# Kernel tuning notes

Measured on AMD Instinct MI355X. Metric: run time of the kernel, lower is better.

Reference implementation:

```python
import jax, jax.numpy as jnp
import numpy as np

N_NODES = 50000
N_EDGES = 800000
NODE_DIM = 64
EDGE_DIM = 16
HIDDEN = 128
EPS = 1e-5


def _linear_init(key, fan_in, fan_out):
    k1, k2 = jax.random.split(key)
    bound = 1.0 / np.sqrt(fan_in)
    W = jax.random.uniform(k1, (fan_in, fan_out), minval=-bound, maxval=bound, dtype=jnp.float32)
    b = jax.random.uniform(k2, (fan_out,), minval=-bound, maxval=bound, dtype=jnp.float32)
    return W, b


def batchnorm(h, gamma, beta):
    # BatchNorm1d in training mode: batch mean/var (biased), eps=1e-5
    mu = jnp.mean(h, axis=0, keepdims=True)
    var = jnp.mean((h - mu) ** 2, axis=0, keepdims=True)
    return (h - mu) * jax.lax.rsqrt(var + EPS) * gamma + beta


def setup_inputs() -> dict:
    key = jax.random.key(0)
    ks = jax.random.split(key, 8)
    x = jax.random.normal(ks[0], (N_NODES, NODE_DIM), dtype=jnp.float32)
    edge_index = jax.random.randint(ks[1], (2, N_EDGES), 0, N_NODES, dtype=jnp.int64)
    edge_attr = jax.random.normal(ks[2], (N_EDGES, EDGE_DIM), dtype=jnp.float32)
    We1, be1 = _linear_init(ks[3], 2 * NODE_DIM + EDGE_DIM, HIDDEN)
    We2, be2 = _linear_init(ks[4], HIDDEN, HIDDEN)
    Wm, bm = _linear_init(ks[5], HIDDEN, HIDDEN)
    Wn1, bn1 = _linear_init(ks[6], NODE_DIM + HIDDEN, HIDDEN)
    Wn2, bn2 = _linear_init(ks[7], HIDDEN, HIDDEN)
    ones = jnp.ones((HIDDEN,), jnp.float32)
    zeros = jnp.zeros((HIDDEN,), jnp.float32)
    return dict(x=x, edge_index=edge_index, edge_attr=edge_attr,
                We1=We1, be1=be1, ge=ones, bbe=zeros, We2=We2, be2=be2,
                Wm=Wm, bm=bm,
                Wn1=Wn1, bn1=bn1, gn=ones, bbn=zeros, Wn2=Wn2, bn2=bn2)


def reference(x, edge_index, edge_attr, We1, be1, ge, bbe, We2, be2, Wm, bm, Wn1, bn1, gn, bbn, Wn2, bn2):
    row, col = edge_index[0], edge_index[1]
    # gather + concat -> edge network (Linear, BN, ReLU, Linear)
    edge_input = jnp.concatenate([x[row], x[col], edge_attr], axis=-1)  # [E, 2n+e]
    h = jax.nn.relu(batchnorm(edge_input @ We1 + be1, ge, bbe))
    edge_features = h @ We2 + be2
    # message MLP (Linear, ReLU)
    messages = jax.nn.relu(edge_features @ Wm + bm)  # [E, H]
    # scatter-add into source nodes
    agg = jax.ops.segment_sum(messages, row, num_segments=N_NODES)  # [N, H]
    # node network (Linear, BN, ReLU, Linear)
    node_input = jnp.concatenate([x, agg], axis=-1)
    hn = jax.nn.relu(batchnorm(node_input @ Wn1 + bn1, gn, bbn))
    return hn @ Wn2 + bn2
```

## Files before the change

### kernel.cpp

```cpp
#include <hip/hip_runtime.h>
#include <stdint.h>

#define NNODES 50000
#define NEDGES 800000
#define H 128
#define BN_EPS 1e-5f

typedef short short8 __attribute__((ext_vector_type(8)));
typedef short short4v __attribute__((ext_vector_type(4)));
typedef float f32x4 __attribute__((ext_vector_type(4)));

__device__ __forceinline__ float bf2f(unsigned short u) {
    unsigned int v = ((unsigned int)u) << 16;
    return __uint_as_float(v);
}
__device__ __forceinline__ unsigned short f2bf(float f) {
    unsigned int x = __float_as_uint(f);
    return (unsigned short)((x + 0x7FFFu + ((x >> 16) & 1u)) >> 16);
}
__device__ __forceinline__ short8 s8z() { short8 z = {0,0,0,0,0,0,0,0}; return z; }

template<int KB>
__device__ __forceinline__ void gemm_tile(const short* __restrict__ sA, const int SK,
                                          const unsigned short* __restrict__ WT, const int RK,
                                          const int n0, f32x4 acc[4][4], const int lane) {
    const int mr = lane & 15, quad = lane >> 4;
    const short* W = (const short*)WT;
    #pragma unroll
    for (int kb = 0; kb < KB; ++kb) {
        short8 a[4];
        #pragma unroll
        for (int mt = 0; mt < 4; ++mt)
            a[mt] = *(const short8*)&sA[(mt*16 + mr)*SK + kb*32 + quad*8];
        #pragma unroll
        for (int nt = 0; nt < 4; ++nt) {
            short8 b = *(const short8*)&W[(size_t)(n0 + nt*16 + mr)*RK + kb*32 + quad*8];
            #pragma unroll
            for (int mt = 0; mt < 4; ++mt)
                acc[mt][nt] = __builtin_amdgcn_mfma_f32_16x16x32_bf16(a[mt], b, acc[mt][nt], 0, 0, 0);
        }
    }
}

__global__ void k_fold(const float* __restrict__ We2, const float* __restrict__ be2,
                       const float* __restrict__ Wm, const float* __restrict__ bm,
                       float* __restrict__ W2m, float* __restrict__ b2m) {
    int j = threadIdx.x;
    int i = blockIdx.x;
    if (i < H) {
        float acc = 0.f;
        for (int k = 0; k < H; ++k) acc = fmaf(We2[i*H + k], Wm[k*H + j], acc);
        W2m[i*H + j] = acc;
    } else {
        float acc = bm[j];
        for (int k = 0; k < H; ++k) acc = fmaf(be2[k], Wm[k*H + j], acc);
        b2m[j] = acc;
    }
}

__global__ void k_prep2(const float* __restrict__ We1, const float* __restrict__ Wn1,
                        const float* __restrict__ Wn2,
                        unsigned short* __restrict__ WabT, unsigned short* __restrict__ Wn1T,
                        unsigned short* __restrict__ Wn2T, unsigned short* __restrict__ WcT,
                        int* __restrict__ cnt, float* __restrict__ S1f) {
    int i = blockIdx.x*256 + threadIdx.x;
    if (i < 16384) {
        int n = i >> 6, k = i & 63;
        WabT[n*64 + k] = f2bf(We1[(n < 128 ? k : 64 + k)*H + (n & 127)]);
    } else if (i < 40960) {
        int j = i - 16384; int n = j / 192, k = j - n*192;
        Wn1T[n*192 + k] = f2bf(Wn1[k*H + n]);
    } else if (i < 57344) {
        int j = i - 40960; int n = j >> 7, k = j & 127;
        Wn2T[n*H + k] = f2bf(Wn2[k*H + n]);
    } else if (i < 61440) {
        int j = i - 57344; int n = j >> 5, k = j & 31;
        WcT[n*32 + k] = (k < 16) ? f2bf(We1[(128 + k)*H + n]) : (unsigned short)0;
    } else if (i < 111440) {
        cnt[i - 61440] = 0;
    } else if (i < 112464) {
        S1f[i - 111440] = 0.f;
    }
}

__global__ void k_count(const int* __restrict__ ei, int* __restrict__ cnt) {
    int e = blockIdx.x*256 + threadIdx.x;
    if (e < NEDGES) atomicAdd(&cnt[ei[e]], 1);
}

__global__ void k_scanA(const int* __restrict__ cnt, int* __restrict__ bsum) {
    __shared__ int ws[4];
    const int tid = threadIdx.x;
    int i = blockIdx.x*256 + tid;
    int v = (i < NNODES) ? cnt[i] : 0;
    #pragma unroll
    for (int off = 32; off > 0; off >>= 1) v += __shfl_down(v, off);
    if ((tid & 63) == 0) ws[tid >> 6] = v;
    __syncthreads();
    if (tid == 0) bsum[blockIdx.x] = ws[0] + ws[1] + ws[2] + ws[3];
}

__global__ void k_scanB(const int* __restrict__ bsum, int* __restrict__ bpre,
                        int* __restrict__ offsets) {
    __shared__ int ws[4];
    const int tid = threadIdx.x;
    const int lane = tid & 63, wid = tid >> 6;
    int v = (tid < 196) ? bsum[tid] : 0;
    int xv = v;
    #pragma unroll
    for (int off = 1; off < 64; off <<= 1) {
        int y = __shfl_up(xv, off);
        if (lane >= off) xv += y;
    }
    if (lane == 63) ws[wid] = xv;
    __syncthreads();
    int base = 0;
    for (int w = 0; w < 4; ++w) if (w < wid) base += ws[w];
    int incl = base + xv;
    if (tid < 196) bpre[tid] = incl - v;
    if (tid == 255) offsets[NNODES] = incl;
}

__global__ void k_scanC(const int* __restrict__ cnt, const int* __restrict__ bpre,
                        int* __restrict__ offsets, int* __restrict__ cursor) {
    __shared__ int ws[4];
    const int tid = threadIdx.x;
    const int lane = tid & 63, wid = tid >> 6;
    int i = blockIdx.x*256 + tid;
    int v = (i < NNODES) ? cnt[i] : 0;
    int xv = v;
    #pragma unroll
    for (int off = 1; off < 64; off <<= 1) {
        int y = __shfl_up(xv, off);
        if (lane >= off) xv += y;
    }
    if (lane == 63) ws[wid] = xv;
    __syncthreads();
    int base = bpre[blockIdx.x];
    for (int w = 0; w < 4; ++w) if (w < wid) base += ws[w];
    int excl = base + xv - v;
    if (i < NNODES) { offsets[i] = excl; cursor[i] = excl; }
}

__global__ void k_scatter(const int* __restrict__ ei, int* __restrict__ cursor,
                          int* __restrict__ elist) {
    int e = blockIdx.x*256 + threadIdx.x;
    if (e < NEDGES) {
        int p = atomicAdd(&cursor[ei[e]], 1);
        elist[p] = e;
    }
}

__launch_bounds__(256)
__global__ void k_T(const float* __restrict__ x, const unsigned short* __restrict__ WabT,
                    unsigned short* __restrict__ T) {
    __shared__ short sA[128*72];
    const int tid = threadIdx.x;
    const int n0b = blockIdx.x*128;
    {
        const int rowl = tid >> 1, half = (tid & 1)*32;
        const int node = n0b + rowl;
        const bool ok = node < NNODES;
        #pragma unroll
        for (int c = 0; c < 4; ++c) {
            int k0 = half + c*8;
            short8 o = s8z();
            if (ok) {
                float4 a = *(const float4*)&x[node*64 + k0];
                float4 b = *(const float4*)&x[node*64 + k0 + 4];
                o[0]=(short)f2bf(a.x); o[1]=(short)f2bf(a.y); o[2]=(short)f2bf(a.z); o[3]=(short)f2bf(a.w);
                o[4]=(short)f2bf(b.x); o[5]=(short)f2bf(b.y); o[6]=(short)f2bf(b.z); o[7]=(short)f2bf(b.w);
            }
            *(short8*)&sA[rowl*72 + k0] = o;
        }
    }
    __syncthreads();
    const int wave = tid >> 6, lane = tid & 63;
    const int m0 = (wave & 1)*64;
    const int n0 = blockIdx.y*128 + (wave >> 1)*64;
    f32x4 acc[4][4];
    f32x4 z = {0.f, 0.f, 0.f, 0.f};
    #pragma unroll
    for (int mt = 0; mt < 4; ++mt)
        #pragma unroll
        for (int nt = 0; nt < 4; ++nt) acc[mt][nt] = z;
    gemm_tile<2>(sA + m0*72, 72, WabT, 64, n0, acc, lane);
    const int mr = lane & 15, quad = lane >> 4;
    #pragma unroll
    for (int nt = 0; nt < 4; ++nt) {
        int j = n0 + nt*16 + mr;
        #pragma unroll
        for (int mt = 0; mt < 4; ++mt) {
            int nb = n0b + m0 + mt*16 + quad*4;
            #pragma unroll
            for (int r = 0; r < 4; ++r) {
                int node = nb + r;
                if (node < NNODES) T[(size_t)node*256 + j] = f2bf(acc[mt][nt][r]);
            }
        }
    }
}

__launch_bounds__(256, 4)
__global__ void k_gather3(const unsigned short* __restrict__ T, const int* __restrict__ ei,
                          const int* __restrict__ elist, const float* __restrict__ ea,
                          const unsigned short* __restrict__ WcT, const float* __restrict__ be1,
                          unsigned short* __restrict__ hb,
                          float* __restrict__ gS, float* __restrict__ gSS) {
    __shared__ short sT[128*136];
    __shared__ float sS[H], sSS[H];
    const int tid = threadIdx.x;
    const int p0 = blockIdx.x*128;
    const int wave = tid >> 6, lane = tid & 63;
    const int mr = lane & 15, quad = lane >> 4;
    const int mbase = wave*32;
    if (tid < 128) { sS[tid] = 0.f; sSS[tid] = 0.f; }
    const int lp = tid >> 1, half = tid & 1;
    const int e = elist[p0 + lp];
    const bool eaActive = (quad < 2);
    int e0i = 0, e1i = 0;
    if (eaActive) {
        e0i = elist[p0 + mbase + mr];
        e1i = elist[p0 + mbase + 16 + mr];
    }
    const int row = ei[e], col = ei[NEDGES + e];
    f32x4 u0, u1, v0, v1;
    if (eaActive) {
        u0 = __builtin_nontemporal_load((const f32x4*)&ea[(size_t)e0i*16 + quad*8]);
        u1 = __builtin_nontemporal_load((const f32x4*)&ea[(size_t)e0i*16 + quad*8 + 4]);
        v0 = __builtin_nontemporal_load((const f32x4*)&ea[(size_t)e1i*16 + quad*8]);
        v1 = __builtin_nontemporal_load((const f32x4*)&ea[(size_t)e1i*16 + quad*8 + 4]);
    }
    const unsigned short* Tr = &T[(size_t)row*256 + half*64];
    const unsigned short* Tc = &T[(size_t)col*256 + 128 + half*64];
    short8 t1[8], t2[8];
    #pragma unroll
    for (int c = 0; c < 8; ++c) t1[c] = *(const short8*)&Tr[c*8];
    #pragma unroll
    for (int c = 0; c < 8; ++c) t2[c] = *(const short8*)&Tc[c*8];
    __builtin_amdgcn_sched_barrier(0);
    short8 a0 = s8z(), a1 = s8z();
    if (eaActive) {
        a0[0]=(short)f2bf(u0[0]); a0[1]=(short)f2bf(u0[1]); a0[2]=(short)f2bf(u0[2]); a0[3]=(short)f2bf(u0[3]);
        a0[4]=(short)f2bf(u1[0]); a0[5]=(short)f2bf(u1[1]); a0[6]=(short)f2bf(u1[2]); a0[7]=(short)f2bf(u1[3]);
        a1[0]=(short)f2bf(v0[0]); a1[1]=(short)f2bf(v0[1]); a1[2]=(short)f2bf(v0[2]); a1[3]=(short)f2bf(v0[3]);
        a1[4]=(short)f2bf(v1[0]); a1[5]=(short)f2bf(v1[1]); a1[6]=(short)f2bf(v1[2]); a1[7]=(short)f2bf(v1[3]);
    }
    #pragma unroll
    for (int c = 0; c < 8; ++c) {
        short8 o;
        #pragma unroll
        for (int i = 0; i < 8; ++i)
            o[i] = (short)f2bf(bf2f((unsigned short)t1[c][i]) + bf2f((unsigned short)t2[c][i]));
        *(short8*)&sT[lp*136 + half*64 + c*8] = o;
    }
    f32x4 acc[2][8];
    f32x4 z = {0.f, 0.f, 0.f, 0.f};
    #pragma unroll
    for (int mt = 0; mt < 2; ++mt)
        #pragma unroll
        for (int nt = 0; nt < 8; ++nt) acc[mt][nt] = z;
    #pragma unroll
    for (int nt = 0; nt < 8; ++nt) {
        short8 b = *(const short8*)&WcT[(nt*16 + mr)*32 + quad*8];
        acc[0][nt] = __builtin_amdgcn_mfma_f32_16x16x32_bf16(a0, b, acc[0][nt], 0, 0, 0);
        acc[1][nt] = __builtin_amdgcn_mfma_f32_16x16x32_bf16(a1, b, acc[1][nt], 0, 0, 0);
    }
    __syncthreads();
    #pragma unroll
    for (int nt = 0; nt < 8; ++nt) {
        int j = nt*16 + mr;
        float bia = be1[j];
        float s = 0.f, ssum = 0.f;
        #pragma unroll
        for (int mt = 0; mt < 2; ++mt) {
            #pragma unroll
            for (int r = 0; r < 4; ++r) {
                int m = mbase + mt*16 + quad*4 + r;
                float v = acc[mt][nt][r] + bf2f((unsigned short)sT[m*136 + j]) + bia;
                sT[m*136 + j] = (short)f2bf(v);
                s += v; ssum += v*v;
            }
        }
        s += __shfl_xor(s, 16);
        ssum += __shfl_xor(ssum, 16);
        s += __shfl_xor(s, 32);
        ssum += __shfl_xor(ssum, 32);
        if (quad == 0) {
            atomicAdd(&sS[j], s);
            atomicAdd(&sSS[j], ssum);
        }
    }
    __syncthreads();
    #pragma unroll
    for (int c = 0; c < 8; ++c) {
        int k0 = half*64 + c*8;
        int kb = k0 >> 5, quadS = (k0 >> 3) & 3;
        short8 v = *(const short8*)&sT[lp*136 + k0];
        __builtin_nontemporal_store(v,
            (short8*)&hb[((size_t)(blockIdx.x*16 + kb*4 + quadS)*128 + lp)*8]);
    }
    if (tid < 128) { atomicAdd(&gS[tid], sS[tid]); atomicAdd(&gSS[tid], sSS[tid]); }
}

__global__ void k_stats(const float* __restrict__ S, const float* __restrict__ SS,
                        const float* __restrict__ g, const float* __restrict__ b,
                        float invCount, float* __restrict__ scale, float* __restrict__ shift) {
    int j = threadIdx.x;
    float mu = S[j]*invCount;
    float var = SS[j]*invCount - mu*mu;
    float sc = rsqrtf(var + BN_EPS)*g[j];
    scale[j] = sc;
    shift[j] = b[j] - mu*sc;
}

__global__ void k_prep3(const float* __restrict__ W2m, const float* __restrict__ scale,
                        const float* __restrict__ shift, unsigned short* __restrict__ W2mST,
                        float* __restrict__ tvec, float* __restrict__ agg) {
    int i = blockIdx.x*256 + threadIdx.x;
    if (i < 16384) {
        int n = i >> 7, k = i & 127;
        W2mST[n*H + k] = f2bf(scale[k] * W2m[k*H + n]);
    } else if (i < 16512) {
        int k = i - 16384;
        tvec[k] = shift[k] / scale[k];
    } else if (i < 16512 + NNODES*H) {
        agg[i - 16512] = 0.f;
    }
}

__launch_bounds__(256)
__global__ void k_msgagg(const unsigned short* __restrict__ hb, const float* __restrict__ tvec,
                         const unsigned short* __restrict__ W2mST, const float* __restrict__ b2m,
                         const int* __restrict__ ei, const int* __restrict__ elist,
                         const int* __restrict__ offsets, float* __restrict__ agg) {
    __shared__ short sA[128*136];
    __shared__ int rows[128];
    __shared__ int segStart[130];
    __shared__ int wcnt[2];
    __shared__ int nsegS;
    const int tid = threadIdx.x;
    const int p0 = blockIdx.x*128;
    const int wave = tid >> 6, lane = tid & 63;
    const int mr = lane & 15, quad = lane >> 4;
    const int mbase = wave*32;
    short8 raw[4][2];
    #pragma unroll
    for (int kb = 0; kb < 4; ++kb)
        #pragma unroll
        for (int mt = 0; mt < 2; ++mt)
            raw[kb][mt] = __builtin_nontemporal_load(
                (const short8*)&hb[((size_t)(blockIdx.x*16 + kb*4 + quad)*128
                                    + mbase + mt*16 + mr)*8]);
    int pre = 0, st = 0;
    if (tid < 128) rows[tid] = ei[elist[p0 + tid]];
    __syncthreads();
    if (tid < 128) {
        int r0 = rows[tid];
        st = (tid == 0) || (rows[tid - 1] != r0);
        unsigned long long m = __ballot(st);
        int lane2 = tid & 63;
        pre = __popcll(m & ((1ull << lane2) - 1ull));
        if (lane2 == 63) wcnt[tid >> 6] = pre + st;
    }
    __syncthreads();
    if (tid < 128) {
        int base = (tid >= 64) ? wcnt[0] : 0;
        int sid = base + pre + st - 1;
        if (st) segStart[sid] = tid;
        if (tid == 127) {
            int ns = wcnt[0] + wcnt[1];
            nsegS = ns;
            segStart[ns] = 128;
        }
    }
    f32x4 acc[2][8];
    f32x4 z = {0.f, 0.f, 0.f, 0.f};
    #pragma unroll
    for (int mt = 0; mt < 2; ++mt)
        #pragma unroll
        for (int nt = 0; nt < 8; ++nt) acc[mt][nt] = z;
    #pragma unroll
    for (int kb = 0; kb < 4; ++kb) {
        float4 tq0 = *(const float4*)&tvec[kb*32 + quad*8];
        float4 tq1 = *(const float4*)&tvec[kb*32 + quad*8 + 4];
        short8 a[2];
        #pragma unroll
        for (int mt = 0; mt < 2; ++mt) {
            short8 rw = raw[kb][mt];
            short8 av;
            av[0] = (short)f2bf(fmaxf(bf2f((unsigned short)rw[0]) + tq0.x, 0.f));
            av[1] = (short)f2bf(fmaxf(bf2f((unsigned short)rw[1]) + tq0.y, 0.f));
            av[2] = (short)f2bf(fmaxf(bf2f((unsigned short)rw[2]) + tq0.z, 0.f));
            av[3] = (short)f2bf(fmaxf(bf2f((unsigned short)rw[3]) + tq0.w, 0.f));
            av[4] = (short)f2bf(fmaxf(bf2f((unsigned short)rw[4]) + tq1.x, 0.f));
            av[5] = (short)f2bf(fmaxf(bf2f((unsigned short)rw[5]) + tq1.y, 0.f));
            av[6] = (short)f2bf(fmaxf(bf2f((unsigned short)rw[6]) + tq1.z, 0.f));
            av[7] = (short)f2bf(fmaxf(bf2f((unsigned short)rw[7]) + tq1.w, 0.f));
            a[mt] = av;
        }
        #pragma unroll
        for (int nt = 0; nt < 8; ++nt) {
            short8 b = *(const short8*)&W2mST[(nt*16 + mr)*H + kb*32 + quad*8];
            acc[0][nt] = __builtin_amdgcn_mfma_f32_16x16x32_bf16(a[0], b, acc[0][nt], 0, 0, 0);
            acc[1][nt] = __builtin_amdgcn_mfma_f32_16x16x32_bf16(a[1], b, acc[1][nt], 0, 0, 0);
        }
    }
    #pragma unroll
    for (int nt = 0; nt < 8; ++nt) {
        int j = nt*16 + mr;
        float bias = b2m[j];
        #pragma unroll
        for (int mt = 0; mt < 2; ++mt) {
            #pragma unroll
            for (int r = 0; r < 4; ++r) {
                int m = mbase + mt*16 + quad*4 + r;
                sA[m*136 + j] = (short)f2bf(fmaxf(acc[mt][nt][r] + bias, 0.f));
            }
        }
    }
    __syncthreads();
    const int nseg = nsegS;
    for (int idx = tid; idx < (nseg << 5); idx += 256) {
        int s = idx >> 5, g = idx & 31;
        int j0 = g*4;
        int a0 = segStart[s], b0 = segStart[s + 1];
        float s0 = 0.f, s1 = 0.f, s2 = 0.f, s3 = 0.f;
        for (int i = a0; i < b0; ++i) {
            short4v v = *(const short4v*)&sA[i*136 + j0];
            s0 += bf2f((unsigned short)v[0]);
            s1 += bf2f((unsigned short)v[1]);
            s2 += bf2f((unsigned short)v[2]);
            s3 += bf2f((unsigned short)v[3]);
        }
        int r = rows[a0];
        bool interior = (a0 > 0) && (b0 < 128);
        bool full = interior || ((p0 + a0 == offsets[r]) && (p0 + b0 == offsets[r + 1]));
        float* dst = &agg[(size_t)r*H + j0];
        if (full) {
            f32x4 o = {s0, s1, s2, s3};
            *(f32x4*)dst = o;
        } else {
            atomicAdd(dst + 0, s0);
            atomicAdd(dst + 1, s1);
            atomicAdd(dst + 2, s2);
            atomicAdd(dst + 3, s3);
        }
    }
}

__launch_bounds__(256)
__global__ void k_node1(const float* __restrict__ x, const float* __restrict__ agg,
                        const unsigned short* __restrict__ Wn1T, const float* __restrict__ bn1,
                        float* __restrict__ h2, float* __restrict__ gS, float* __restrict__ gSS) {
    __shared__ short sA[128*200];
    __shared__ float sS[H], sSS[H];
    const int tid = threadIdx.x;
    if (tid < H) { sS[tid] = 0.f; sSS[tid] = 0.f; }
    const int n0b = blockIdx.x*128;
    {
        const int rowl = tid >> 1, half = (tid & 1)*96;
        const int node = n0b + rowl;
        const bool ok = node < NNODES;
        #pragma unroll
        for (int c = 0; c < 12; ++c) {
            int k0 = half + c*8;
            short8 o = s8z();
            if (ok) {
                float4 a, b;
                if (k0 < 64) {
                    a = *(const float4*)&x[node*64 + k0];
                    b = *(const float4*)&x[node*64 + k0 + 4];
                } else {
                    a = *(const float4*)&agg[(size_t)node*H + (k0 - 64)];
                    b = *(const float4*)&agg[(size_t)node*H + (k0 - 64) + 4];
                }
                o[0]=(short)f2bf(a.x); o[1]=(short)f2bf(a.y); o[2]=(short)f2bf(a.z); o[3]=(short)f2bf(a.w);
                o[4]=(short)f2bf(b.x); o[5]=(short)f2bf(b.y); o[6]=(short)f2bf(b.z); o[7]=(short)f2bf(b.w);
            }
            *(short8*)&sA[rowl*200 + k0] = o;
        }
    }
    __syncthreads();
    const int wave = tid >> 6, lane = tid & 63;
    const int m0 = (wave & 1)*64, n0 = (wave >> 1)*64;
    f32x4 acc[4][4];
    f32x4 z = {0.f, 0.f, 0.f, 0.f};
    #pragma unroll
    for (int mt = 0; mt < 4; ++mt)
        #pragma unroll
        for (int nt = 0; nt < 4; ++nt) acc[mt][nt] = z;
    gemm_tile<6>(sA + m0*200, 200, Wn1T, 192, n0, acc, lane);
    const int mr = lane & 15, quad = lane >> 4;
    #pragma unroll
    for (int nt = 0; nt < 4; ++nt) {
        int j = n0 + nt*16 + mr;
        float bias = bn1[j];
        float s = 0.f, ssum = 0.f;
        #pragma unroll
        for (int mt = 0; mt < 4; ++mt) {
            int nb = n0b + m0 + mt*16 + quad*4;
            #pragma unroll
            for (int r = 0; r < 4; ++r) {
                int node = nb + r;
                if (node < NNODES) {
                    float v = acc[mt][nt][r] + bias;
                    h2[(size_t)node*H + j] = v;
                    s += v; ssum += v*v;
                }
            }
        }
        atomicAdd(&sS[j], s);
        atomicAdd(&sSS[j], ssum);
    }
    __syncthreads();
    if (tid < H) { atomicAdd(&gS[tid], sS[tid]); atomicAdd(&gSS[tid], sSS[tid]); }
}

__launch_bounds__(256)
__global__ void k_node2(const float* __restrict__ h2, const float* __restrict__ scale,
                        const float* __restrict__ shift, const unsigned short* __restrict__ Wn2T,
                        const float* __restrict__ bn2, float* __restrict__ out) {
    __shared__ short sA[128*136];
    const int tid = threadIdx.x;
    const int n0b = blockIdx.x*128;
    {
        const int rowl = tid >> 1, half = (tid & 1)*64;
        const int node = n0b + rowl;
        const bool ok = node < NNODES;
        #pragma unroll
        for (int c = 0; c < 8; ++c) {
            int k0 = half + c*8;
            short8 o = s8z();
            if (ok) {
                float4 a = *(const float4*)&h2[(size_t)node*H + k0];
                float4 b = *(const float4*)&h2[(size_t)node*H + k0 + 4];
                float4 sc0 = *(const float4*)&scale[k0], sc1 = *(const float4*)&scale[k0 + 4];
                float4 sh0 = *(const float4*)&shift[k0], sh1 = *(const float4*)&shift[k0 + 4];
                o[0] = (short)f2bf(fmaxf(fmaf(a.x, sc0.x, sh0.x), 0.f));
                o[1] = (short)f2bf(fmaxf(fmaf(a.y, sc0.y, sh0.y), 0.f));
                o[2] = (short)f2bf(fmaxf(fmaf(a.z, sc0.z, sh0.z), 0.f));
                o[3] = (short)f2bf(fmaxf(fmaf(a.w, sc0.w, sh0.w), 0.f));
                o[4] = (short)f2bf(fmaxf(fmaf(b.x, sc1.x, sh1.x), 0.f));
                o[5] = (short)f2bf(fmaxf(fmaf(b.y, sc1.y, sh1.y), 0.f));
                o[6] = (short)f2bf(fmaxf(fmaf(b.z, sc1.z, sh1.z), 0.f));
                o[7] = (short)f2bf(fmaxf(fmaf(b.w, sc1.w, sh1.w), 0.f));
            }
            *(short8*)&sA[rowl*136 + k0] = o;
        }
    }
    __syncthreads();
    const int wave = tid >> 6, lane = tid & 63;
    const int m0 = (wave & 1)*64, n0 = (wave >> 1)*64;
    f32x4 acc[4][4];
    f32x4 z = {0.f, 0.f, 0.f, 0.f};
    #pragma unroll
    for (int mt = 0; mt < 4; ++mt)
        #pragma unroll
        for (int nt = 0; nt < 4; ++nt) acc[mt][nt] = z;
    gemm_tile<4>(sA + m0*136, 136, Wn2T, 128, n0, acc, lane);
    const int mr = lane & 15, quad = lane >> 4;
    #pragma unroll
    for (int nt = 0; nt < 4; ++nt) {
        int j = n0 + nt*16 + mr;
        float bias = bn2[j];
        #pragma unroll
        for (int mt = 0; mt < 4; ++mt) {
            int nb = n0b + m0 + mt*16 + quad*4;
            #pragma unroll
            for (int r = 0; r < 4; ++r) {
                int node = nb + r;
                if (node < NNODES) out[(size_t)node*H + j] = acc[mt][nt][r] + bias;
            }
        }
    }
}

extern "C" void kernel_launch(void* const* d_in, const int* in_sizes, int n_in,
                              void* d_out, int out_size, void* d_ws, size_t ws_size,
                              hipStream_t stream) {
    (void)in_sizes; (void)n_in; (void)out_size; (void)ws_size;
    const float* x   = (const float*)d_in[0];
    const int*   ei  = (const int*)d_in[1];
    const float* ea  = (const float*)d_in[2];
    const float* We1 = (const float*)d_in[3];
    const float* be1 = (const float*)d_in[4];
    const float* ge  = (const float*)d_in[5];
    const float* bbe = (const float*)d_in[6];
    const float* We2 = (const float*)d_in[7];
    const float* be2 = (const float*)d_in[8];
    const float* Wm  = (const float*)d_in[9];
    const float* bm  = (const float*)d_in[10];
    const float* Wn1 = (const float*)d_in[11];
    const float* bn1 = (const float*)d_in[12];
    const float* gn  = (const float*)d_in[13];
    const float* bbn = (const float*)d_in[14];
    const float* Wn2 = (const float*)d_in[15];
    const float* bn2 = (const float*)d_in[16];
    float* out = (float*)d_out;

    char* ws = (char*)d_ws;
    unsigned short* hb   = (unsigned short*)(ws);
    float*          h2   = (float*)(ws);
    float*          agg  = (float*)(ws + 204800000);
    unsigned short* Tbuf = (unsigned short*)(ws + 230400000);
    int* cnt     = (int*)(ws + 256000000);
    int* offsets = (int*)(ws + 256200192);
    int* cursor  = (int*)(ws + 256400448);
    int* bsum    = (int*)(ws + 256600448);
    int* bpre    = (int*)(ws + 256601472);
    int* elist   = (int*)(ws + 256602496);
    float* S1     = (float*)(ws + 259802496);
    float* SS1    = S1 + 128;
    float* S2     = S1 + 256;
    float* SS2    = S1 + 384;
    float* scale1 = S1 + 512;
    float* shift1 = S1 + 640;
    float* scale2 = S1 + 768;
    float* shift2 = S1 + 896;
    float* W2m  = (float*)(ws + 259806592);
    float* b2m  = (float*)(ws + 259872128);
    float* tvec = (float*)(ws + 259872640);
    unsigned short* WabT  = (unsigned short*)(ws + 259873152);
    unsigned short* Wn1T  = (unsigned short*)(ws + 259905920);
    unsigned short* Wn2T  = (unsigned short*)(ws + 259955072);
    unsigned short* W2mST = (unsigned short*)(ws + 259987840);
    unsigned short* WcT   = (unsigned short*)(ws + 260020608);

    k_fold<<<H + 1, H, 0, stream>>>(We2, be2, Wm, bm, W2m, b2m);
    k_prep2<<<440, 256, 0, stream>>>(We1, Wn1, Wn2, WabT, Wn1T, Wn2T, WcT, cnt, S1);
    k_count<<<NEDGES/256, 256, 0, stream>>>(ei, cnt);
    k_scanA<<<196, 256, 0, stream>>>(cnt, bsum);
    k_scanB<<<1, 256, 0, stream>>>(bsum, bpre, offsets);
    k_scanC<<<196, 256, 0, stream>>>(cnt, bpre, offsets, cursor);
    k_scatter<<<NEDGES/256, 256, 0, stream>>>(ei, cursor, elist);
    k_T<<<dim3(391, 2), 256, 0, stream>>>(x, WabT, Tbuf);
    k_gather3<<<NEDGES/128, 256, 0, stream>>>(Tbuf, ei, elist, ea, WcT, be1, hb, S1, SS1);
    k_stats<<<1, H, 0, stream>>>(S1, SS1, ge, bbe, 1.0f/NEDGES, scale1, shift1);
    k_prep3<<<12565, 256, 0, stream>>>(W2m, scale1, shift1, W2mST, tvec, agg);
    k_msgagg<<<NEDGES/128, 256, 0, stream>>>(hb, tvec, W2mST, b2m, ei, elist, offsets, agg);
    k_node1<<<391, 256, 0, stream>>>(x, agg, Wn1T, bn1, h2, S2, SS2);
    k_stats<<<1, H, 0, stream>>>(S2, SS2, gn, bbn, 1.0f/NNODES, scale2, shift2);
    k_node2<<<391, 256, 0, stream>>>(h2, scale2, shift2, Wn2T, bn2, out);
}
```

Measured before the change: 655.2 us.

## Recompute edge hidden activations in second pass instead of storing them

The first edge pass now only computes batch-norm statistics and saves edge attributes as compact bf16, no longer writing the full 128-wide hidden activation buffer. The message/aggregation pass re-gathers the per-node projections, redoes the edge-attribute MFMA and bias add, and feeds the result straight into the message GEMM from shared memory. This trades a large write plus read of the E×128 intermediate for a second random gather of node rows and repeated compute. The second kernel also gets a tighter launch bound and higher register pressure.

Result: no change. 658.3 us (+0.5%).

```diff
diff --git a/kernel.cpp b/kernel.cpp
--- a/kernel.cpp
+++ b/kernel.cpp
@@ -202,11 +202,11 @@
 }
 
 __launch_bounds__(256, 4)
-__global__ void k_gather3(const unsigned short* __restrict__ T, const int* __restrict__ ei,
-                          const int* __restrict__ elist, const float* __restrict__ ea,
-                          const unsigned short* __restrict__ WcT, const float* __restrict__ be1,
-                          unsigned short* __restrict__ hb,
-                          float* __restrict__ gS, float* __restrict__ gSS) {
+__global__ void k_pass1(const unsigned short* __restrict__ T, const int* __restrict__ ei,
+                        const int* __restrict__ elist, const float* __restrict__ ea,
+                        const unsigned short* __restrict__ WcT, const float* __restrict__ be1,
+                        unsigned short* __restrict__ eaP,
+                        float* __restrict__ gS, float* __restrict__ gSS) {
     __shared__ short sT[128*136];
     __shared__ float sS[H], sSS[H];
     const int tid = threadIdx.x;
@@ -245,6 +245,8 @@
         a0[4]=(short)f2bf(u1[0]); a0[5]=(short)f2bf(u1[1]); a0[6]=(short)f2bf(u1[2]); a0[7]=(short)f2bf(u1[3]);
         a1[0]=(short)f2bf(v0[0]); a1[1]=(short)f2bf(v0[1]); a1[2]=(short)f2bf(v0[2]); a1[3]=(short)f2bf(v0[3]);
         a1[4]=(short)f2bf(v1[0]); a1[5]=(short)f2bf(v1[1]); a1[6]=(short)f2bf(v1[2]); a1[7]=(short)f2bf(v1[3]);
+        *(short8*)&eaP[(size_t)(p0 + mbase + mr)*16 + quad*8] = a0;
+        *(short8*)&eaP[(size_t)(p0 + mbase + 16 + mr)*16 + quad*8] = a1;
     }
     #pragma unroll
     for (int c = 0; c < 8; ++c) {
@@ -278,7 +280,6 @@
             for (int r = 0; r < 4; ++r) {
                 int m = mbase + mt*16 + quad*4 + r;
                 float v = acc[mt][nt][r] + bf2f((unsigned short)sT[m*136 + j]) + bia;
-                sT[m*136 + j] = (short)f2bf(v);
                 s += v; ssum += v*v;
             }
         }
@@ -292,14 +293,6 @@
         }
     }
     __syncthreads();
-    #pragma unroll
-    for (int c = 0; c < 8; ++c) {
-        int k0 = half*64 + c*8;
-        int kb = k0 >> 5, quadS = (k0 >> 3) & 3;
-        short8 v = *(const short8*)&sT[lp*136 + k0];
-        __builtin_nontemporal_store(v,
-            (short8*)&hb[((size_t)(blockIdx.x*16 + kb*4 + quadS)*128 + lp)*8]);
-    }
     if (tid < 128) { atomicAdd(&gS[tid], sS[tid]); atomicAdd(&gSS[tid], sSS[tid]); }
 }
 
@@ -329,12 +322,14 @@
     }
 }
 
-__launch_bounds__(256)
-__global__ void k_msgagg(const unsigned short* __restrict__ hb, const float* __restrict__ tvec,
-                         const unsigned short* __restrict__ W2mST, const float* __restrict__ b2m,
-                         const int* __restrict__ ei, const int* __restrict__ elist,
-                         const int* __restrict__ offsets, float* __restrict__ agg) {
-    __shared__ short sA[128*136];
+__launch_bounds__(256, 4)
+__global__ void k_pass2(const unsigned short* __restrict__ T, const int* __restrict__ ei,
+                        const int* __restrict__ elist, const unsigned short* __restrict__ eaP,
+                        const unsigned short* __restrict__ WcT, const float* __restrict__ be1,
+                        const float* __restrict__ tvec, const unsigned short* __restrict__ W2mST,
+                        const float* __restrict__ b2m, const int* __restrict__ offsets,
+                        float* __restrict__ agg) {
+    __shared__ short sT[128*136];
     __shared__ int rows[128];
     __shared__ int segStart[130];
     __shared__ int wcnt[2];
@@ -344,17 +339,45 @@
     const int wave = tid >> 6, lane = tid & 63;
     const int mr = lane & 15, quad = lane >> 4;
     const int mbase = wave*32;
-    short8 raw[4][2];
-    #pragma unroll
-    for (int kb = 0; kb < 4; ++kb)
-        #pragma unroll
-        for (int mt = 0; mt < 2; ++mt)
-            raw[kb][mt] = __builtin_nontemporal_load(
-                (const short8*)&hb[((size_t)(blockIdx.x*16 + kb*4 + quad)*128
-                                    + mbase + mt*16 + mr)*8]);
+    const int lp = tid >> 1, half = tid & 1;
+    const int e = elist[p0 + lp];
+    const int row = ei[e], col = ei[NEDGES + e];
+    if (half == 0) rows[lp] = row;
+    short8 a0 = s8z(), a1 = s8z();
+    if (quad < 2) {
+        a0 = *(const short8*)&eaP[(size_t)(p0 + mbase + mr)*16 + quad*8];
+        a1 = *(const short8*)&eaP[(size_t)(p0 + mbase + 16 + mr)*16 + quad*8];
+    }
+    const unsigned short* Tr = &T[(size_t)row*256 + half*64];
+    const unsigned short* Tc = &T[(size_t)col*256 + 128 + half*64];
+    short8 t1[8], t2[8];
+    #pragma unroll
+    for (int c = 0; c < 8; ++c) t1[c] = *(const short8*)&Tr[c*8];
+    #pragma unroll
+    for (int c = 0; c < 8; ++c) t2[c] = *(const short8*)&Tc[c*8];
+    __builtin_amdgcn_sched_barrier(0);
+    #pragma unroll
+    for (int c = 0; c < 8; ++c) {
+        short8 o;
+        #pragma unroll
+        for (int i = 0; i < 8; ++i)
+            o[i] = (short)f2bf(bf2f((unsigned short)t1[c][i]) + bf2f((unsigned short)t2[c][i]));
+        *(short8*)&sT[lp*136 + half*64 + c*8] = o;
+    }
+    f32x4 accE[2][8];
+    f32x4 z = {0.f, 0.f, 0.f, 0.f};
+    #pragma unroll
+    for (int mt = 0; mt < 2; ++mt)
+        #pragma unroll
+        for (int nt = 0; nt < 8; ++nt) accE[mt][nt] = z;
+    #pragma unroll
+    for (int nt = 0; nt < 8; ++nt) {
+        short8 b = *(const short8*)&WcT[(nt*16 + mr)*32 + quad*8];
+        accE[0][nt] = __builtin_amdgcn_mfma_f32_16x16x32_bf16(a0, b, accE[0][nt], 0, 0, 0);
+        accE[1][nt] = __builtin_amdgcn_mfma_f32_16x16x32_bf16(a1, b, accE[1][nt], 0, 0, 0);
+    }
+    __syncthreads();
     int pre = 0, st = 0;
-    if (tid < 128) rows[tid] = ei[elist[p0 + tid]];
-    __syncthreads();
     if (tid < 128) {
         int r0 = rows[tid];
         st = (tid == 0) || (rows[tid - 1] != r0);
@@ -374,8 +397,27 @@
             segStart[ns] = 128;
         }
     }
+    #pragma unroll
+    for (int nt = 0; nt < 8; ++nt) {
+        int j = nt*16 + mr;
+        float bia = be1[j];
+        #pragma unroll
+        for (int mt = 0; mt < 2; ++mt) {
+            #pragma unroll
+            for (int r = 0; r < 4; ++r) {
+                int m = mbase + mt*16 + quad*4 + r;
+                float v = accE[mt][nt][r] + bf2f((unsigned short)sT[m*136 + j]) + bia;
+                sT[m*136 + j] = (short)f2bf(v);
+            }
+        }
+    }
+    short8 raw[4][2];
+    #pragma unroll
+    for (int kb = 0; kb < 4; ++kb)
+        #pragma unroll
+        for (int mt = 0; mt < 2; ++mt)
+            raw[kb][mt] = *(const short8*)&sT[(mbase + mt*16 + mr)*136 + kb*32 + quad*8];
     f32x4 acc[2][8];
-    f32x4 z = {0.f, 0.f, 0.f, 0.f};
     #pragma unroll
     for (int mt = 0; mt < 2; ++mt)
         #pragma unroll
@@ -415,7 +457,7 @@
             #pragma unroll
             for (int r = 0; r < 4; ++r) {
                 int m = mbase + mt*16 + quad*4 + r;
-                sA[m*136 + j] = (short)f2bf(fmaxf(acc[mt][nt][r] + bias, 0.f));
+                sT[m*136 + j] = (short)f2bf(fmaxf(acc[mt][nt][r] + bias, 0.f));
             }
         }
     }
@@ -424,18 +466,18 @@
     for (int idx = tid; idx < (nseg << 5); idx += 256) {
         int s = idx >> 5, g = idx & 31;
         int j0 = g*4;
-        int a0 = segStart[s], b0 = segStart[s + 1];
+        int a0s = segStart[s], b0s = segStart[s + 1];
         float s0 = 0.f, s1 = 0.f, s2 = 0.f, s3 = 0.f;
-        for (int i = a0; i < b0; ++i) {
-            short4v v = *(const short4v*)&sA[i*136 + j0];
+        for (int i = a0s; i < b0s; ++i) {
+            short4v v = *(const short4v*)&sT[i*136 + j0];
             s0 += bf2f((unsigned short)v[0]);
             s1 += bf2f((unsigned short)v[1]);
             s2 += bf2f((unsigned short)v[2]);
             s3 += bf2f((unsigned short)v[3]);
         }
-        int r = rows[a0];
-        bool interior = (a0 > 0) && (b0 < 128);
-        bool full = interior || ((p0 + a0 == offsets[r]) && (p0 + b0 == offsets[r + 1]));
+        int r = rows[a0s];
+        bool interior = (a0s > 0) && (b0s < 128);
+        bool full = interior || ((p0 + a0s == offsets[r]) && (p0 + b0s == offsets[r + 1]));
         float* dst = &agg[(size_t)r*H + j0];
         if (full) {
             f32x4 o = {s0, s1, s2, s3};
@@ -600,7 +642,7 @@
     float* out = (float*)d_out;
 
     char* ws = (char*)d_ws;
-    unsigned short* hb   = (unsigned short*)(ws);
+    unsigned short* eaP  = (unsigned short*)(ws);
     float*          h2   = (float*)(ws);
     float*          agg  = (float*)(ws + 204800000);
     unsigned short* Tbuf = (unsigned short*)(ws + 230400000);
@@ -635,10 +677,11 @@
     k_scanC<<<196, 256, 0, stream>>>(cnt, bpre, offsets, cursor);
     k_scatter<<<NEDGES/256, 256, 0, stream>>>(ei, cursor, elist);
     k_T<<<dim3(391, 2), 256, 0, stream>>>(x, WabT, Tbuf);
-    k_gather3<<<NEDGES/128, 256, 0, stream>>>(Tbuf, ei, elist, ea, WcT, be1, hb, S1, SS1);
+    k_pass1<<<NEDGES/128, 256, 0, stream>>>(Tbuf, ei, elist, ea, WcT, be1, eaP, S1, SS1);
     k_stats<<<1, H, 0, stream>>>(S1, SS1, ge, bbe, 1.0f/NEDGES, scale1, shift1);
     k_prep3<<<12565, 256, 0, stream>>>(W2m, scale1, shift1, W2mST, tvec, agg);
-    k_msgagg<<<NEDGES/128, 256, 0, stream>>>(hb, tvec, W2mST, b2m, ei, elist, offsets, agg);
+    k_pass2<<<NEDGES/128, 256, 0, stream>>>(Tbuf, ei, elist, eaP, WcT, be1, tvec, W2mST,
+                                            b2m, offsets, agg);
     k_node1<<<391, 256, 0, stream>>>(x, agg, Wn1T, bn1, h2, S2, SS2);
     k_stats<<<1, H, 0, stream>>>(S2, SS2, gn, bbn, 1.0f/NNODES, scale2, shift2);
     k_node2<<<391, 256, 0, stream>>>(h2, scale2, shift2, Wn2T, bn2, out);
```
